# Optimization experiments

Measured on AMD Instinct MI355X. Metric: run time of the kernel, lower is better.

The kernel has to match this reference:

```python
import jax, jax.numpy as jnp
from jax import lax
import numpy as np

DG = 2          # deformable groups
KH = KW = 3     # kernel size
KK = KH * KW
PAD = 1


def setup_inputs() -> dict:
    key = jax.random.key(0)
    k1, k2, k3 = jax.random.split(key, 3)
    B, C, H, W = 4, 64, 128, 128
    O = 64
    x = jax.random.normal(k1, (B, C, H, W), jnp.float32)
    # original inits offset weights to 0 (degenerate: plain conv); use small random
    # weights instead so the irregular bilinear-gather path is actually exercised.
    w_off = jax.random.normal(k2, (DG * 2 * KK, C, KH, KW), jnp.float32) * 0.05
    w_def = jax.random.normal(k3, (O, C, KH, KW), jnp.float32) * (1.0 / np.sqrt(C * KK))
    return {"x": x, "w_off": w_off, "w_def": w_def}


def _deform_conv(x, w_off, w_def):
    B, C, H, W = x.shape
    O = w_def.shape[0]
    Cg = C // DG

    # offset = offset_conv(x): stride 1, pad 1, no bias -> [B, DG*2*KK, H, W]
    offset = lax.conv_general_dilated(
        x, w_off, window_strides=(1, 1), padding=((PAD, PAD), (PAD, PAD)),
        dimension_numbers=("NCHW", "OIHW", "NCHW"))
    # DCN layout: per group, per kernel tap k, channel 2k = dy, 2k+1 = dx
    off = offset.reshape(B, DG, KK, 2, H, W)

    ki, kj = jnp.meshgrid(jnp.arange(KH), jnp.arange(KW), indexing="ij")
    ki = (ki.reshape(KK) - PAD).astype(x.dtype)   # kernel row offsets -1..1
    kj = (kj.reshape(KK) - PAD).astype(x.dtype)
    hh = jnp.arange(H, dtype=x.dtype)
    ww = jnp.arange(W, dtype=x.dtype)

    # sampling positions [B, DG, KK, H, W]
    py = off[:, :, :, 0] + ki[None, None, :, None, None] + hh[None, None, None, :, None]
    px = off[:, :, :, 1] + kj[None, None, :, None, None] + ww[None, None, None, None, :]

    y0 = jnp.floor(py).astype(jnp.int32)
    x0 = jnp.floor(px).astype(jnp.int32)
    dy = py - y0.astype(x.dtype)
    dx = px - x0.astype(x.dtype)

    x_g = x.reshape(B, DG, Cg, H * W)

    def gather(yi, xi):
        # zero padding outside the image
        valid = ((yi >= 0) & (yi < H) & (xi >= 0) & (xi < W)).astype(x.dtype)
        yc = jnp.clip(yi, 0, H - 1)
        xc = jnp.clip(xi, 0, W - 1)
        idx = (yc * W + xc).reshape(B, DG, 1, KK * H * W)
        v = jnp.take_along_axis(x_g, idx, axis=3).reshape(B, DG, Cg, KK, H, W)
        return v * valid[:, :, None]  # broadcast over channel axis

    # bilinear interpolation at learned offset positions
    val = (gather(y0, x0) * ((1 - dy) * (1 - dx))[:, :, None]
           + gather(y0, x0 + 1) * ((1 - dy) * dx)[:, :, None]
           + gather(y0 + 1, x0) * (dy * (1 - dx))[:, :, None]
           + gather(y0 + 1, x0 + 1) * (dy * dx)[:, :, None])

    # weighted accumulation: conv groups = 1, channel dim = DG*Cg
    w = w_def.reshape(O, DG, Cg, KK)
    return jnp.einsum("bgckhw,ogck->bohw", val, w)


def reference(x, w_off, w_def):
    return _deform_conv(x, w_off, w_def)
```

## Files before the change

kernel.cpp:

```cpp
#include <hip/hip_runtime.h>
#include <hip/hip_bf16.h>

typedef _Float16 f16x8 __attribute__((ext_vector_type(8)));
typedef _Float16 f16x2 __attribute__((ext_vector_type(2)));
typedef float f32x4  __attribute__((ext_vector_type(4)));

#define Bn 4
#define Cn 64
#define Hn 128
#define Wn 128
#define HWn 16384

#define XT_BYTES    (Bn*HWn*Cn*2)
#define PKDEF_BYTES (18*4*64*8*2)

static __device__ __forceinline__ unsigned pk_f16(float lo, float hi) {
  union { _Float16 h[2]; unsigned u; } cv;
  cv.h[0] = (_Float16)lo; cv.h[1] = (_Float16)hi;
  return cv.u;
}

__global__ __launch_bounds__(256) void transpose_cast(const float* __restrict__ x,
                                                      ushort* __restrict__ xt) {
  __shared__ float tile[64][65];
  const int t = threadIdx.x;
  const int blk = blockIdx.x;
  const int b = blk >> 8;
  const int pix0 = (blk & 255) * 64;
  const int y = pix0 >> 7, x0 = pix0 & 127;
  const float* xb = x + (b * Cn) * HWn + pix0;
#pragma unroll
  for (int q = 0; q < 16; ++q) {
    int idx = q * 256 + t;
    int c = idx >> 6, p = idx & 63;
    tile[c][p] = xb[c * HWn + p];
  }
  __syncthreads();
  const int p = t & 63, cg = t >> 6;
#pragma unroll
  for (int half = 0; half < 2; ++half) {
    const int seg = cg * 2 + half;
    unsigned u[4];
#pragma unroll
    for (int j = 0; j < 4; ++j)
      u[j] = pk_f16(tile[seg * 8 + 2 * j][p], tile[seg * 8 + 2 * j + 1][p]);
    uint4 v = {u[0], u[1], u[2], u[3]};
    *(uint4*)(xt + (((((b << 7) + y) << 3) + seg) * 128 + x0 + p) * 8) = v;
  }
}

__global__ __launch_bounds__(256) void prep_pack(const float* __restrict__ w_off,
                                                 const float* __restrict__ w_def,
                                                 ushort* __restrict__ pk_def,
                                                 ushort* __restrict__ pk_off) {
  const int t = blockIdx.x * 256 + threadIdx.x;
  if (t < 4608) {
    int lane = t & 63, oc = (t >> 6) & 3, s = t >> 8;
    int g = s / 9, k = s % 9;
    int o = oc * 16 + (lane & 15);
    int cb = g * 32 + (lane >> 4) * 8;
    unsigned u[4];
#pragma unroll
    for (int j = 0; j < 4; ++j)
      u[j] = pk_f16(w_def[(o * Cn + cb + 2 * j) * 9 + k],
                    w_def[(o * Cn + cb + 2 * j + 1) * 9 + k]);
    uint4 v = {u[0], u[1], u[2], u[3]};
    *(uint4*)(pk_def + t * 8) = v;
  } else if (t < 8064) {
    int t2 = t - 4608;
    int lane = t2 & 63, r = t2 >> 6;
    int oc = r % 3, s = r / 3;
    int k = s >> 1, chalf = s & 1;
    int o = oc * 16 + (lane & 15);
    int cb = chalf * 32 + (lane >> 4) * 8;
    unsigned u[4];
#pragma unroll
    for (int j = 0; j < 4; ++j) {
      float lo = (o < 36) ? w_off[(o * Cn + cb + 2 * j) * 9 + k] : 0.f;
      float hi = (o < 36) ? w_off[(o * Cn + cb + 2 * j + 1) * 9 + k] : 0.f;
      u[j] = pk_f16(lo, hi);
    }
    uint4 v = {u[0], u[1], u[2], u[3]};
    *(uint4*)(pk_off + (r * 64 + lane) * 8) = v;
  }
}

#define T_STRIDE (17*24*8)
__global__ __launch_bounds__(1024, 8) void deform_fused(const ushort* __restrict__ xt,
                                                        const ushort* __restrict__ pk_def,
                                                        const ushort* __restrict__ pk_off,
                                                        float* __restrict__ out) {
  __shared__ ushort tile[8 * 17 * 24 * 8];
  __shared__ _Float16 off_lds[8][36][18];
  const int t = threadIdx.x;
  const int lane = t & 63;
  const int wid = t >> 6;
  const int pg = wid >> 1, gsel = wid & 1;
  int bid = blockIdx.x;
  bid = (bid & 7) * 64 + (bid >> 3);
  const int b  = bid >> 7;
  const int ty = (bid >> 3) & 15;
  const int tx = bid & 7;
  const int y0t = ty * 8, x0t = tx * 16;
  const int TLY = max(0, y0t - 4), THY = min(127, y0t + 12);
  const int TLX = max(0, x0t - 3), THX = min(127, x0t + 19);
  const int Hd = THY - TLY + 1, Wd = THX - TLX + 1;

  {
    const int xq = t & 31;
    const int r0 = t >> 5;
    const int nr = Hd * 8;
    for (int rr = r0; rr < nr; rr += 32) {
      const int yq = rr >> 3, seg = rr & 7;
      if (xq < Wd) {
        const ushort* src = xt + ((((b << 7) + TLY + yq) << 3) + seg) * 1024 + (TLX + xq) * 8;
        *(uint4*)&tile[seg * T_STRIDE + (yq * 24 + xq) * 8] = *(const uint4*)src;
      }
    }
  }
  __syncthreads();

  const int h = y0t + pg;
  const int p = lane & 15, kq = lane >> 4;
  const int w_ = x0t + p;
  const int pixin = (h << 7) + x0t;
  const int su = gsel * 4 + kq;
  const int colb = lane & 15;

  int pixoff[9]; bool tvalid[9];
#pragma unroll
  for (int kk = 0; kk < 9; ++kk) {
    int yk = h + kk / 3 - 1, xk = w_ + kk % 3 - 1;
    tvalid[kk] = ((unsigned)yk < 128u) && ((unsigned)xk < 128u);
    int yc = min(max(yk, 0), 127), xc = min(max(xk, 0), 127);
    pixoff[kk] = ((yc - TLY) * 24 + (xc - TLX)) * 8;
  }

  {
    f32x4 oa0 = {0,0,0,0}, oa1 = {0,0,0,0}, oa2 = {0,0,0,0};
    const f16x8* pBo = (const f16x8*)pk_off;
#pragma unroll
    for (int s = 0; s < 18; ++s) {
      const int k = s >> 1, chalf = s & 1;
      uint4 t_ = *(const uint4*)&tile[(chalf * 4 + kq) * T_STRIDE + pixoff[k]];
      if (!tvalid[k]) { t_.x = 0; t_.y = 0; t_.z = 0; t_.w = 0; }
      union { uint4 u; f16x8 v; } A; A.u = t_;
      if (gsel == 0) {
        oa0 = __builtin_amdgcn_mfma_f32_16x16x32_f16(A.v, pBo[(s*3 + 0)*64 + lane], oa0, 0,0,0);
      } else {
        oa1 = __builtin_amdgcn_mfma_f32_16x16x32_f16(A.v, pBo[(s*3 + 1)*64 + lane], oa1, 0,0,0);
        oa2 = __builtin_amdgcn_mfma_f32_16x16x32_f16(A.v, pBo[(s*3 + 2)*64 + lane], oa2, 0,0,0);
      }
    }
    if (gsel == 0) {
#pragma unroll
      for (int r = 0; r < 4; ++r) off_lds[pg][colb][kq * 4 + r] = (_Float16)oa0[r];
    } else {
#pragma unroll
      for (int r = 0; r < 4; ++r) {
        off_lds[pg][16 + colb][kq * 4 + r] = (_Float16)oa1[r];
        if (colb < 4) off_lds[pg][32 + colb][kq * 4 + r] = (_Float16)oa2[r];
      }
    }
  }
  __syncthreads();

  float offv[18];
#pragma unroll
  for (int j = 0; j < 18; ++j) offv[j] = (float)off_lds[pg][gsel * 18 + j][p];

  f32x4 acc0={0,0,0,0}, acc1={0,0,0,0}, acc2={0,0,0,0}, acc3={0,0,0,0};
  const f16x8* pB = (const f16x8*)pk_def;

#pragma unroll
  for (int j = 0; j < 9; ++j) {
    const int k = j;
    float py = offv[2*j]   + (float)(h  + k / 3 - 1);
    float px = offv[2*j+1] + (float)(w_ + k % 3 - 1);
    float fy = floorf(py), fx = floorf(px);
    int y0 = (int)fy, x0 = (int)fx;
    float dy = py - fy, dx = px - fx;

    bool vy0 = (y0 >= 0) && (y0 < Hn);
    bool vy1 = (y0 >= -1) && (y0 < Hn - 1);
    bool vx0 = (x0 >= 0) && (x0 < Wn);
    bool vx1 = (x0 >= -1) && (x0 < Wn - 1);
    float omdy = 1.f - dy, omdx = 1.f - dx;
    float w00 = (vy0 && vx0) ? omdy * omdx : 0.f;
    float w01 = (vy0 && vx1) ? omdy * dx   : 0.f;
    float w10 = (vy1 && vx0) ? dy * omdx   : 0.f;
    float w11 = (vy1 && vx1) ? dy * dx     : 0.f;

    int iy0 = min(max(y0, 0), Hn - 1), iy1 = min(max(y0 + 1, 0), Hn - 1);
    int ix0 = min(max(x0, 0), Wn - 1), ix1 = min(max(x0 + 1, 0), Wn - 1);

    uint4 c00, c01, c10, c11;
    bool intile = (iy0 >= TLY) && (iy1 <= THY) && (ix0 >= TLX) && (ix1 <= THX);
    if (__all((int)intile)) {
      const int base = su * T_STRIDE;
      const int ly0 = iy0 - TLY, ly1 = iy1 - TLY;
      const int lx0 = ix0 - TLX, lx1 = ix1 - TLX;
      c00 = *(const uint4*)&tile[base + (ly0 * 24 + lx0) * 8];
      c01 = *(const uint4*)&tile[base + (ly0 * 24 + lx1) * 8];
      c10 = *(const uint4*)&tile[base + (ly1 * 24 + lx0) * 8];
      c11 = *(const uint4*)&tile[base + (ly1 * 24 + lx1) * 8];
    } else {
      const int r0g = ((((b << 7) + iy0) << 3) + su) * 128;
      const int r1g = ((((b << 7) + iy1) << 3) + su) * 128;
      c00 = *(const uint4*)(xt + (r0g + ix0) * 8);
      c01 = *(const uint4*)(xt + (r0g + ix1) * 8);
      c10 = *(const uint4*)(xt + (r1g + ix0) * 8);
      c11 = *(const uint4*)(xt + (r1g + ix1) * 8);
    }

    const _Float16 h00 = (_Float16)w00, h01 = (_Float16)w01;
    const _Float16 h10 = (_Float16)w10, h11 = (_Float16)w11;
    const f16x2 W00 = {h00, h00}, W01 = {h01, h01};
    const f16x2 W10 = {h10, h10}, W11 = {h11, h11};
    union U32H { unsigned u; f16x2 h; };
    union { uint4 u; f16x8 v; } A;
#define BILC(comp, fld)                                                        \
    { U32H a0, a1, a2, a3, r;                                                  \
      a0.u = c00.comp; a1.u = c01.comp; a2.u = c10.comp; a3.u = c11.comp;      \
      r.h = a0.h * W00 + a1.h * W01 + a2.h * W10 + a3.h * W11;                 \
      A.u.fld = r.u; }
    BILC(x, x) BILC(y, y) BILC(z, z) BILC(w, w)
#undef BILC

    const int s = gsel * 9 + j;
    acc0 = __builtin_amdgcn_mfma_f32_16x16x32_f16(A.v, pB[(s*4 + 0)*64 + lane], acc0, 0,0,0);
    acc1 = __builtin_amdgcn_mfma_f32_16x16x32_f16(A.v, pB[(s*4 + 1)*64 + lane], acc1, 0,0,0);
    acc2 = __builtin_amdgcn_mfma_f32_16x16x32_f16(A.v, pB[(s*4 + 2)*64 + lane], acc2, 0,0,0);
    acc3 = __builtin_amdgcn_mfma_f32_16x16x32_f16(A.v, pB[(s*4 + 3)*64 + lane], acc3, 0,0,0);
  }

  __syncthreads();
  float* red = (float*)tile;
  if (gsel == 1) {
    *(f32x4*)&red[((pg * 4 + 0) * 64 + lane) * 4] = acc0;
    *(f32x4*)&red[((pg * 4 + 1) * 64 + lane) * 4] = acc1;
    *(f32x4*)&red[((pg * 4 + 2) * 64 + lane) * 4] = acc2;
    *(f32x4*)&red[((pg * 4 + 3) * 64 + lane) * 4] = acc3;
  }
  __syncthreads();
  if (gsel == 0) {
    acc0 += *(const f32x4*)&red[((pg * 4 + 0) * 64 + lane) * 4];
    acc1 += *(const f32x4*)&red[((pg * 4 + 1) * 64 + lane) * 4];
    acc2 += *(const f32x4*)&red[((pg * 4 + 2) * 64 + lane) * 4];
    acc3 += *(const f32x4*)&red[((pg * 4 + 3) * 64 + lane) * 4];
    float* ob = out + pixin + kq * 4;
#pragma unroll
    for (int r = 0; r < 4; ++r) {
      ob[((b*64 +      colb) << 14) + r] = acc0[r];
      ob[((b*64 + 16 + colb) << 14) + r] = acc1[r];
      ob[((b*64 + 32 + colb) << 14) + r] = acc2[r];
      ob[((b*64 + 48 + colb) << 14) + r] = acc3[r];
    }
  }
}

extern "C" void kernel_launch(void* const* d_in, const int* in_sizes, int n_in,
                              void* d_out, int out_size, void* d_ws, size_t ws_size,
                              hipStream_t stream) {
  const float* x     = (const float*)d_in[0];
  const float* w_off = (const float*)d_in[1];
  const float* w_def = (const float*)d_in[2];
  float* out = (float*)d_out;

  char* ws = (char*)d_ws;
  ushort* xt     = (ushort*)ws;
  ushort* pk_def = (ushort*)(ws + XT_BYTES);
  ushort* pk_off = (ushort*)(ws + XT_BYTES + PKDEF_BYTES);

  transpose_cast<<<1024, 256, 0, stream>>>(x, xt);
  prep_pack<<<32, 256, 0, stream>>>(w_off, w_def, pk_def, pk_off);
  deform_fused<<<512, 1024, 0, stream>>>(xt, pk_def, pk_off, out);
}
```

Before: 49.94 us.

## Merge prep kernels, vectorize transpose loads, pad LDS, split reduction across wave pairs

Merges the transpose/cast and weight-packing kernels into a single launch, which removes one kernel launch and its gap. The transpose now loads with float4 and pads the shared tile to reduce bank conflicts. The deform kernel's LDS tile stride is padded, MFMA issue is bracketed with s_setprio, and the final cross-wave reduction and store are split so both wave groups each reduce and write half the outputs. These are several independent micro-optimizations; the padding increases LDS usage, which may affect occupancy.

```diff
diff --git a/kernel.cpp b/kernel.cpp
--- a/kernel.cpp
+++ b/kernel.cpp
@@ -20,77 +20,79 @@
   return cv.u;
 }
 
-__global__ __launch_bounds__(256) void transpose_cast(const float* __restrict__ x,
-                                                      ushort* __restrict__ xt) {
-  __shared__ float tile[64][65];
+__global__ __launch_bounds__(256) void prep_all(const float* __restrict__ x,
+                                                const float* __restrict__ w_off,
+                                                const float* __restrict__ w_def,
+                                                ushort* __restrict__ xt,
+                                                ushort* __restrict__ pk_def,
+                                                ushort* __restrict__ pk_off) {
+  __shared__ float tile[64][68];
   const int t = threadIdx.x;
   const int blk = blockIdx.x;
-  const int b = blk >> 8;
-  const int pix0 = (blk & 255) * 64;
-  const int y = pix0 >> 7, x0 = pix0 & 127;
-  const float* xb = x + (b * Cn) * HWn + pix0;
-#pragma unroll
-  for (int q = 0; q < 16; ++q) {
-    int idx = q * 256 + t;
-    int c = idx >> 6, p = idx & 63;
-    tile[c][p] = xb[c * HWn + p];
-  }
-  __syncthreads();
-  const int p = t & 63, cg = t >> 6;
-#pragma unroll
-  for (int half = 0; half < 2; ++half) {
-    const int seg = cg * 2 + half;
-    unsigned u[4];
-#pragma unroll
-    for (int j = 0; j < 4; ++j)
-      u[j] = pk_f16(tile[seg * 8 + 2 * j][p], tile[seg * 8 + 2 * j + 1][p]);
-    uint4 v = {u[0], u[1], u[2], u[3]};
-    *(uint4*)(xt + (((((b << 7) + y) << 3) + seg) * 128 + x0 + p) * 8) = v;
-  }
-}
-
-__global__ __launch_bounds__(256) void prep_pack(const float* __restrict__ w_off,
-                                                 const float* __restrict__ w_def,
-                                                 ushort* __restrict__ pk_def,
-                                                 ushort* __restrict__ pk_off) {
-  const int t = blockIdx.x * 256 + threadIdx.x;
-  if (t < 4608) {
-    int lane = t & 63, oc = (t >> 6) & 3, s = t >> 8;
-    int g = s / 9, k = s % 9;
-    int o = oc * 16 + (lane & 15);
-    int cb = g * 32 + (lane >> 4) * 8;
-    unsigned u[4];
-#pragma unroll
-    for (int j = 0; j < 4; ++j)
-      u[j] = pk_f16(w_def[(o * Cn + cb + 2 * j) * 9 + k],
-                    w_def[(o * Cn + cb + 2 * j + 1) * 9 + k]);
-    uint4 v = {u[0], u[1], u[2], u[3]};
-    *(uint4*)(pk_def + t * 8) = v;
-  } else if (t < 8064) {
-    int t2 = t - 4608;
-    int lane = t2 & 63, r = t2 >> 6;
-    int oc = r % 3, s = r / 3;
-    int k = s >> 1, chalf = s & 1;
-    int o = oc * 16 + (lane & 15);
-    int cb = chalf * 32 + (lane >> 4) * 8;
-    unsigned u[4];
-#pragma unroll
-    for (int j = 0; j < 4; ++j) {
-      float lo = (o < 36) ? w_off[(o * Cn + cb + 2 * j) * 9 + k] : 0.f;
-      float hi = (o < 36) ? w_off[(o * Cn + cb + 2 * j + 1) * 9 + k] : 0.f;
-      u[j] = pk_f16(lo, hi);
-    }
-    uint4 v = {u[0], u[1], u[2], u[3]};
-    *(uint4*)(pk_off + (r * 64 + lane) * 8) = v;
-  }
-}
-
-#define T_STRIDE (17*24*8)
+  if (blk < 1024) {
+    const int b = blk >> 8;
+    const int pix0 = (blk & 255) * 64;
+    const int y = pix0 >> 7, x0 = pix0 & 127;
+    const float* xb = x + (b * Cn) * HWn + pix0;
+#pragma unroll
+    for (int q = 0; q < 4; ++q) {
+      int idx = q * 256 + t;
+      int c = idx >> 4, p4 = idx & 15;
+      float4 v = *(const float4*)(xb + c * HWn + p4 * 4);
+      *(float4*)&tile[c][p4 * 4] = v;
+    }
+    __syncthreads();
+    const int p = t & 63, cg = t >> 6;
+#pragma unroll
+    for (int half = 0; half < 2; ++half) {
+      const int seg = cg * 2 + half;
+      unsigned u[4];
+#pragma unroll
+      for (int j = 0; j < 4; ++j)
+        u[j] = pk_f16(tile[seg * 8 + 2 * j][p], tile[seg * 8 + 2 * j + 1][p]);
+      uint4 v = {u[0], u[1], u[2], u[3]};
+      *(uint4*)(xt + (((((b << 7) + y) << 3) + seg) * 128 + x0 + p) * 8) = v;
+    }
+  } else {
+    const int tt = (blk - 1024) * 256 + t;
+    if (tt < 4608) {
+      int lane = tt & 63, oc = (tt >> 6) & 3, s = tt >> 8;
+      int g = s / 9, k = s % 9;
+      int o = oc * 16 + (lane & 15);
+      int cb = g * 32 + (lane >> 4) * 8;
+      unsigned u[4];
+#pragma unroll
+      for (int j = 0; j < 4; ++j)
+        u[j] = pk_f16(w_def[(o * Cn + cb + 2 * j) * 9 + k],
+                      w_def[(o * Cn + cb + 2 * j + 1) * 9 + k]);
+      uint4 v = {u[0], u[1], u[2], u[3]};
+      *(uint4*)(pk_def + tt * 8) = v;
+    } else if (tt < 8064) {
+      int t2 = tt - 4608;
+      int lane = t2 & 63, r = t2 >> 6;
+      int oc = r % 3, s = r / 3;
+      int k = s >> 1, chalf = s & 1;
+      int o = oc * 16 + (lane & 15);
+      int cb = chalf * 32 + (lane >> 4) * 8;
+      unsigned u[4];
+#pragma unroll
+      for (int j = 0; j < 4; ++j) {
+        float lo = (o < 36) ? w_off[(o * Cn + cb + 2 * j) * 9 + k] : 0.f;
+        float hi = (o < 36) ? w_off[(o * Cn + cb + 2 * j + 1) * 9 + k] : 0.f;
+        u[j] = pk_f16(lo, hi);
+      }
+      uint4 v = {u[0], u[1], u[2], u[3]};
+      *(uint4*)(pk_off + (r * 64 + lane) * 8) = v;
+    }
+  }
+}
+
+#define T_STRIDE (17*24*8 + 16)
 __global__ __launch_bounds__(1024, 8) void deform_fused(const ushort* __restrict__ xt,
                                                         const ushort* __restrict__ pk_def,
                                                         const ushort* __restrict__ pk_off,
                                                         float* __restrict__ out) {
-  __shared__ ushort tile[8 * 17 * 24 * 8];
+  __shared__ ushort tile[8 * T_STRIDE];
   __shared__ _Float16 off_lds[8][36][18];
   const int t = threadIdx.x;
   const int lane = t & 63;
@@ -228,10 +230,12 @@
 #undef BILC
 
     const int s = gsel * 9 + j;
+    __builtin_amdgcn_s_setprio(1);
     acc0 = __builtin_amdgcn_mfma_f32_16x16x32_f16(A.v, pB[(s*4 + 0)*64 + lane], acc0, 0,0,0);
     acc1 = __builtin_amdgcn_mfma_f32_16x16x32_f16(A.v, pB[(s*4 + 1)*64 + lane], acc1, 0,0,0);
     acc2 = __builtin_amdgcn_mfma_f32_16x16x32_f16(A.v, pB[(s*4 + 2)*64 + lane], acc2, 0,0,0);
     acc3 = __builtin_amdgcn_mfma_f32_16x16x32_f16(A.v, pB[(s*4 + 3)*64 + lane], acc3, 0,0,0);
+    __builtin_amdgcn_s_setprio(0);
   }
 
   __syncthreads();
@@ -239,20 +243,25 @@
   if (gsel == 1) {
     *(f32x4*)&red[((pg * 4 + 0) * 64 + lane) * 4] = acc0;
     *(f32x4*)&red[((pg * 4 + 1) * 64 + lane) * 4] = acc1;
+  } else {
     *(f32x4*)&red[((pg * 4 + 2) * 64 + lane) * 4] = acc2;
     *(f32x4*)&red[((pg * 4 + 3) * 64 + lane) * 4] = acc3;
   }
   __syncthreads();
+  float* ob = out + pixin + kq * 4;
   if (gsel == 0) {
     acc0 += *(const f32x4*)&red[((pg * 4 + 0) * 64 + lane) * 4];
     acc1 += *(const f32x4*)&red[((pg * 4 + 1) * 64 + lane) * 4];
-    acc2 += *(const f32x4*)&red[((pg * 4 + 2) * 64 + lane) * 4];
-    acc3 += *(const f32x4*)&red[((pg * 4 + 3) * 64 + lane) * 4];
-    float* ob = out + pixin + kq * 4;
 #pragma unroll
     for (int r = 0; r < 4; ++r) {
       ob[((b*64 +      colb) << 14) + r] = acc0[r];
       ob[((b*64 + 16 + colb) << 14) + r] = acc1[r];
+    }
+  } else {
+    acc2 += *(const f32x4*)&red[((pg * 4 + 2) * 64 + lane) * 4];
+    acc3 += *(const f32x4*)&red[((pg * 4 + 3) * 64 + lane) * 4];
+#pragma unroll
+    for (int r = 0; r < 4; ++r) {
       ob[((b*64 + 32 + colb) << 14) + r] = acc2[r];
       ob[((b*64 + 48 + colb) << 14) + r] = acc3[r];
     }
@@ -272,7 +281,6 @@
   ushort* pk_def = (ushort*)(ws + XT_BYTES);
   ushort* pk_off = (ushort*)(ws + XT_BYTES + PKDEF_BYTES);
 
-  transpose_cast<<<1024, 256, 0, stream>>>(x, xt);
-  prep_pack<<<32, 256, 0, stream>>>(w_off, w_def, pk_def, pk_off);
+  prep_all<<<1056, 256, 0, stream>>>(x, w_off, w_def, xt, pk_def, pk_off);
   deform_fused<<<512, 1024, 0, stream>>>(xt, pk_def, pk_off, out);
 }
```

New measurement: 52.34 us. 1.05x slower.
